# Optimization experiments

Hardware: AMD Instinct MI355X
Metric: run time of the kernel (lower is better)

The kernel has to match this reference:

```python
import jax, jax.numpy as jnp
import numpy as np

B, T, I, H, FUT = 16384, 50, 6, 128, 30


def setup_inputs() -> dict:
    key = jax.random.key(0)
    ks = jax.random.split(key, 10)
    bound = 1.0 / np.sqrt(H)
    u = lambda k, shape: jax.random.uniform(k, shape, jnp.float32, -bound, bound)
    return {
        "history": jax.random.normal(ks[0], (B, T, I), jnp.float32),
        # GRU weights (PyTorch layout: gates stacked [r, z, n])
        "w_ih": u(ks[1], (3 * H, I)),
        "w_hh": u(ks[2], (3 * H, H)),
        "b_ih": u(ks[3], (3 * H,)),
        "b_hh": u(ks[4], (3 * H,)),
        # MLP head: Linear(H,H) -> ReLU -> Linear(H,I)
        "w1": u(ks[5], (H, H)),
        "b1": u(ks[6], (H,)),
        "w2": u(ks[7], (I, H)),
        "b2": u(ks[8], (I,)),
    }


def _gru_cell(h, x, w_ih, w_hh, b_ih, b_hh):
    # PyTorch GRU cell: gates ordered r, z, n
    gi = x @ w_ih.T + b_ih          # (B, 3H)
    gh = h @ w_hh.T + b_hh          # (B, 3H)
    i_r, i_z, i_n = jnp.split(gi, 3, axis=-1)
    h_r, h_z, h_n = jnp.split(gh, 3, axis=-1)
    r = jax.nn.sigmoid(i_r + h_r)
    z = jax.nn.sigmoid(i_z + h_z)
    n = jnp.tanh(i_n + r * h_n)
    return (1.0 - z) * n + z * h


def reference(history, w_ih, w_hh, b_ih, b_hh, w1, b1, w2, b2):
    # --- encode history: scan GRU over time ---
    h0 = jnp.zeros((history.shape[0], H), history.dtype)

    def enc_step(h, x_t):
        return _gru_cell(h, x_t, w_ih, w_hh, b_ih, b_hh), None

    h_last, _ = jax.lax.scan(enc_step, h0, jnp.swapaxes(history, 0, 1))  # (B, H)

    def head(h):
        return jax.nn.relu(h @ w1.T + b1) @ w2.T + b2  # (B, I)

    def dec_step(carry, _):
        h, x = carry
        h = _gru_cell(h, x, w_ih, w_hh, b_ih, b_hh)
        x = head(h)
        return (h, x), x

    x0 = history[:, -1]  # (B, I)
    _, preds = jax.lax.scan(dec_step, (h_last, x0), None, length=FUT)  # (FUT, B, I)
    return jnp.swapaxes(preds, 0, 1)  # (B, FUT, I)
```

## Files before the change

### kernel.cpp

```cpp
#include <hip/hip_runtime.h>

typedef _Float16 half8 __attribute__((ext_vector_type(8)));
typedef float f32x4 __attribute__((ext_vector_type(4)));

#define ROWS 64
#define HP 136
#define HBUFSZ (ROWS * HP)
#define OP 184
#define LOG2E 1.442695041f
#define MFMA(a,b,c) __builtin_amdgcn_mfma_f32_16x16x32_f16((a),(b),(c),0,0,0)

__global__ __launch_bounds__(512, 2)
void traj_gru(const float* __restrict__ history,
              const float* __restrict__ w_ih, const float* __restrict__ w_hh,
              const float* __restrict__ b_ih, const float* __restrict__ b_hh,
              const float* __restrict__ w1, const float* __restrict__ b1,
              const float* __restrict__ w2, const float* __restrict__ b2,
              float* __restrict__ out)
{
    __shared__ __align__(16) _Float16 hbuf[2 * HBUFSZ];
    __shared__ __align__(16) unsigned char xo_u[50 * ROWS * 16];
    __shared__ __align__(16) _Float16 xdec[ROWS * 8];
    __shared__ __align__(16) _Float16 a1s[ROWS * HP];
    __shared__ __align__(16) _Float16 w2f[4 * 4 * 16 * 8];

    _Float16* xhist = (_Float16*)xo_u;
    float*    outs  = (float*)xo_u;

    const int tid  = threadIdx.x;
    const int wave = tid >> 6;
    const int lane = tid & 63;
    const int ln16 = lane & 15;
    const int q    = lane >> 4;
    const int sw   = ln16 & 3;
    const int rowbase = blockIdx.x * ROWS;
    const int cbase = wave * 16;
    const int bblk  = wave >> 1;
    const int colin = ((wave & 1) << 4) | ln16;

    for (int i = tid; i < 2 * HBUFSZ; i += 512) hbuf[i] = (_Float16)0;
    for (int i = tid; i < ROWS * 8; i += 512) xdec[i] = (_Float16)0;
    for (int i = tid; i < 4 * 4 * 16 * 8; i += 512) w2f[i] = (_Float16)0;
    __syncthreads();
    for (int idx = tid; idx < ROWS * 300; idx += 512) {
        int r = idx / 300, rem = idx - r * 300;
        int t = rem / 6, c = rem - t * 6;
        xhist[(t * ROWS + r) * 8 + c] = (_Float16)history[(rowbase + r) * 300 + rem];
    }
    for (int idx = tid; idx < 50 * ROWS; idx += 512) xhist[idx * 8 + 6] = (_Float16)1.0f;
    for (int idx = tid; idx < ROWS; idx += 512)      xdec[idx * 8 + 6] = (_Float16)1.0f;
    for (int idx = tid; idx < 6 * 128; idx += 512) {
        int n = idx >> 7, k = idx & 127;
        int kt = k >> 5, qq = (k >> 3) & 3, j = k & 7;
        w2f[((kt * 4 + qq) * 16 + n) * 8 + j] = (_Float16)w2[n * 128 + k];
    }

    half8 Bh[3][4];
    #pragma unroll
    for (int g = 0; g < 3; ++g) {
        float sc = (g < 2) ? -LOG2E : -2.0f * LOG2E;
        #pragma unroll
        for (int kt = 0; kt < 4; ++kt) {
            int n = g * 128 + cbase + ln16;
            const float* p = w_hh + n * 128 + kt * 32 + q * 8;
            half8 v;
            #pragma unroll
            for (int j = 0; j < 8; ++j) v[j] = (_Float16)(p[j] * sc);
            Bh[g][kt] = v;
        }
    }
    half8 Bi[3];
    #pragma unroll
    for (int g = 0; g < 3; ++g) {
        float sc = (g < 2) ? -LOG2E : -2.0f * LOG2E;
        int n = g * 128 + cbase + ln16;
        half8 v;
        #pragma unroll
        for (int j = 0; j < 8; ++j) v[j] = (_Float16)0.0f;
        if (q == 0) {
            #pragma unroll
            for (int j = 0; j < 6; ++j) v[j] = (_Float16)(w_ih[n * 6 + j] * sc);
            v[6] = (_Float16)((b_ih[n] + (g < 2 ? b_hh[n] : 0.0f)) * sc);
        }
        Bi[g] = v;
    }
    const float bhn = b_hh[256 + cbase + ln16] * (-2.0f * LOG2E);
    half8 Bw1[4];
    #pragma unroll
    for (int kt = 0; kt < 4; ++kt) {
        int n = cbase + ln16;
        const float* p = w1 + n * 128 + kt * 32 + q * 8;
        half8 v;
        #pragma unroll
        for (int j = 0; j < 8; ++j) v[j] = (_Float16)p[j];
        Bw1[kt] = v;
    }
    const float b1r = b1[cbase + ln16];
    const float b2r = (ln16 < 6) ? b2[ln16] : 0.0f;

    float hp[4][4] = {};

    __syncthreads();

    auto gru_step = [&](int p, const _Float16* xp) {
        const _Float16* hb = hbuf + p * HBUFSZ;
        _Float16*       hn = hbuf + (p ^ 1) * HBUFSZ;
        half8 Ah[2][4], Ax[2];
        f32x4 ar[2], az[2], ahh[2], an[2];

        auto loadA = [&](int c, int buf) {
            const _Float16* rp = hb + (c * 16 + ln16) * HP;
            #pragma unroll
            for (int kt = 0; kt < 4; ++kt)
                Ah[buf][kt] = *(const half8*)(rp + ((kt ^ sw) << 5) + q * 8);
            half8 x = {0,0,0,0,0,0,0,0};
            if (q == 0) x = *(const half8*)(xp + (c * 16 + ln16) * 8);
            Ax[buf] = x;
        };
        auto mfmas = [&](int buf) {
            f32x4 r = {0,0,0,0}, z = {0,0,0,0}, hh = {0,0,0,0}, n = {0,0,0,0};
            #pragma unroll
            for (int kt = 0; kt < 4; ++kt) {
                r  = MFMA(Ah[buf][kt], Bh[0][kt], r);
                z  = MFMA(Ah[buf][kt], Bh[1][kt], z);
                hh = MFMA(Ah[buf][kt], Bh[2][kt], hh);
            }
            r = MFMA(Ax[buf], Bi[0], r);
            z = MFMA(Ax[buf], Bi[1], z);
            n = MFMA(Ax[buf], Bi[2], n);
            ar[buf] = r; az[buf] = z; ahh[buf] = hh; an[buf] = n;
        };

        loadA(0, 0); mfmas(0);
        #pragma unroll
        for (int c = 0; c < 4; ++c) {
            const int cb = c & 1;
            if (c < 3) { loadA(c + 1, cb ^ 1); mfmas(cb ^ 1); }
            #pragma unroll
            for (int i = 0; i < 4; ++i) {
                float r = __builtin_amdgcn_rcpf(1.0f + __builtin_amdgcn_exp2f(ar[cb][i]));
                float z = __builtin_amdgcn_rcpf(1.0f + __builtin_amdgcn_exp2f(az[cb][i]));
                float t = an[cb][i] + r * (ahh[cb][i] + bhn);
                float n = 2.0f * __builtin_amdgcn_rcpf(1.0f + __builtin_amdgcn_exp2f(t)) - 1.0f;
                float h = n + z * (hp[c][i] - n);
                hp[c][i] = h;
                hn[(c * 16 + q * 4 + i) * HP + ((bblk ^ i) << 5) + colin] = (_Float16)h;
            }
        }
        __syncthreads();
    };

    auto head_step = [&](int f, int p) {
        const _Float16* hb = hbuf + p * HBUFSZ;
        half8 Ah[2][4];
        f32x4 aa[2];
        auto loadA = [&](int c, int buf) {
            const _Float16* rp = hb + (c * 16 + ln16) * HP;
            #pragma unroll
            for (int kt = 0; kt < 4; ++kt)
                Ah[buf][kt] = *(const half8*)(rp + ((kt ^ sw) << 5) + q * 8);
        };
        auto mfh = [&](int buf) {
            f32x4 a = {0,0,0,0};
            #pragma unroll
            for (int kt = 0; kt < 4; ++kt) a = MFMA(Ah[buf][kt], Bw1[kt], a);
            aa[buf] = a;
        };
        loadA(0, 0); mfh(0);
        #pragma unroll
        for (int c = 0; c < 4; ++c) {
            const int cb = c & 1;
            if (c < 3) { loadA(c + 1, cb ^ 1); mfh(cb ^ 1); }
            #pragma unroll
            for (int i = 0; i < 4; ++i) {
                float v = aa[cb][i] + b1r;
                v = v > 0.0f ? v : 0.0f;
                a1s[(c * 16 + q * 4 + i) * HP + ((bblk ^ i) << 5) + colin] = (_Float16)v;
            }
        }
        __syncthreads();
        if (wave < 4) {
            const _Float16* rp = a1s + (wave * 16 + ln16) * HP;
            f32x4 o = {0,0,0,0};
            #pragma unroll
            for (int kt = 0; kt < 4; ++kt) {
                half8 Aa = *(const half8*)(rp + ((kt ^ sw) << 5) + q * 8);
                half8 Bw = *(const half8*)&w2f[((kt * 4 + q) * 16 + ln16) * 8];
                o = MFMA(Aa, Bw, o);
            }
            if (ln16 < 6) {
                #pragma unroll
                for (int i = 0; i < 4; ++i) {
                    int row = wave * 16 + q * 4 + i;
                    float v = o[i] + b2r;
                    outs[row * OP + f * 6 + ln16] = v;
                    xdec[row * 8 + ln16] = (_Float16)v;
                }
            }
        }
        __syncthreads();
    };

    int p = 0;
    #pragma unroll 1
    for (int t = 0; t < 50; ++t) { gru_step(p, xhist + t * ROWS * 8); p ^= 1; }
    #pragma unroll 1
    for (int f = 0; f < 30; ++f) {
        gru_step(p, f == 0 ? xhist + 49 * ROWS * 8 : xdec);
        p ^= 1;
        head_step(f, p);
    }

    for (int idx = tid; idx < ROWS * 180; idx += 512) {
        int r = idx / 180, j = idx - r * 180;
        out[(rowbase + r) * 180 + j] = outs[r * OP + j];
    }
}

extern "C" void kernel_launch(void* const* d_in, const int* in_sizes, int n_in,
                              void* d_out, int out_size, void* d_ws, size_t ws_size,
                              hipStream_t stream) {
    (void)in_sizes; (void)n_in; (void)d_ws; (void)ws_size; (void)out_size;
    traj_gru<<<dim3(16384 / ROWS), dim3(512), 0, stream>>>(
        (const float*)d_in[0], (const float*)d_in[1], (const float*)d_in[2],
        (const float*)d_in[3], (const float*)d_in[4], (const float*)d_in[5],
        (const float*)d_in[6], (const float*)d_in[7], (const float*)d_in[8],
        (float*)d_out);
}
```

Measured before the change: 282.0 us.

## Shrink LDS footprint, fold biases into accumulators, write outputs directly

Drops the separate a1s buffer and reuses the idle half of the h double buffer for the head activations. Stores history packed at 6 halves per row and moves the GRU biases into the MFMA accumulator initial values. Writes predictions straight to global memory instead of staging them in LDS. Raises the launch-bounds occupancy hint from 2 to 4 blocks. The goal is less LDS use so more blocks fit per CU, but the tighter register budget that hint implies can force spills, and the direct global stores are small and strided.

Result: slower. 909.6 us (+222.5%).

```diff
diff --git a/kernel.cpp b/kernel.cpp
--- a/kernel.cpp
+++ b/kernel.cpp
@@ -2,15 +2,15 @@
 
 typedef _Float16 half8 __attribute__((ext_vector_type(8)));
 typedef float f32x4 __attribute__((ext_vector_type(4)));
+typedef int int4v __attribute__((ext_vector_type(4)));
 
 #define ROWS 64
 #define HP 136
 #define HBUFSZ (ROWS * HP)
-#define OP 184
 #define LOG2E 1.442695041f
 #define MFMA(a,b,c) __builtin_amdgcn_mfma_f32_16x16x32_f16((a),(b),(c),0,0,0)
 
-__global__ __launch_bounds__(512, 2)
+__global__ __launch_bounds__(512, 4)
 void traj_gru(const float* __restrict__ history,
               const float* __restrict__ w_ih, const float* __restrict__ w_hh,
               const float* __restrict__ b_ih, const float* __restrict__ b_hh,
@@ -19,13 +19,9 @@
               float* __restrict__ out)
 {
     __shared__ __align__(16) _Float16 hbuf[2 * HBUFSZ];
-    __shared__ __align__(16) unsigned char xo_u[50 * ROWS * 16];
+    __shared__ __align__(16) _Float16 xhist[50 * ROWS * 6];
     __shared__ __align__(16) _Float16 xdec[ROWS * 8];
-    __shared__ __align__(16) _Float16 a1s[ROWS * HP];
     __shared__ __align__(16) _Float16 w2f[4 * 4 * 16 * 8];
-
-    _Float16* xhist = (_Float16*)xo_u;
-    float*    outs  = (float*)xo_u;
 
     const int tid  = threadIdx.x;
     const int wave = tid >> 6;
@@ -45,10 +41,8 @@
     for (int idx = tid; idx < ROWS * 300; idx += 512) {
         int r = idx / 300, rem = idx - r * 300;
         int t = rem / 6, c = rem - t * 6;
-        xhist[(t * ROWS + r) * 8 + c] = (_Float16)history[(rowbase + r) * 300 + rem];
-    }
-    for (int idx = tid; idx < 50 * ROWS; idx += 512) xhist[idx * 8 + 6] = (_Float16)1.0f;
-    for (int idx = tid; idx < ROWS; idx += 512)      xdec[idx * 8 + 6] = (_Float16)1.0f;
+        xhist[(t * ROWS + r) * 6 + c] = (_Float16)history[(rowbase + r) * 300 + rem];
+    }
     for (int idx = tid; idx < 6 * 128; idx += 512) {
         int n = idx >> 7, k = idx & 127;
         int kt = k >> 5, qq = (k >> 3) & 3, j = k & 7;
@@ -80,10 +74,12 @@
         if (q == 0) {
             #pragma unroll
             for (int j = 0; j < 6; ++j) v[j] = (_Float16)(w_ih[n * 6 + j] * sc);
-            v[6] = (_Float16)((b_ih[n] + (g < 2 ? b_hh[n] : 0.0f)) * sc);
         }
         Bi[g] = v;
     }
+    const float brr = (b_ih[      cbase + ln16] + b_hh[      cbase + ln16]) * (-LOG2E);
+    const float brz = (b_ih[128 + cbase + ln16] + b_hh[128 + cbase + ln16]) * (-LOG2E);
+    const float bin = b_ih[256 + cbase + ln16] * (-2.0f * LOG2E);
     const float bhn = b_hh[256 + cbase + ln16] * (-2.0f * LOG2E);
     half8 Bw1[4];
     #pragma unroll
@@ -102,7 +98,7 @@
 
     __syncthreads();
 
-    auto gru_step = [&](int p, const _Float16* xp) {
+    auto gru_step = [&](int p, int t, bool enc) {
         const _Float16* hb = hbuf + p * HBUFSZ;
         _Float16*       hn = hbuf + (p ^ 1) * HBUFSZ;
         half8 Ah[2][4], Ax[2];
@@ -114,11 +110,21 @@
             for (int kt = 0; kt < 4; ++kt)
                 Ah[buf][kt] = *(const half8*)(rp + ((kt ^ sw) << 5) + q * 8);
             half8 x = {0,0,0,0,0,0,0,0};
-            if (q == 0) x = *(const half8*)(xp + (c * 16 + ln16) * 8);
+            if (q == 0) {
+                if (enc) {
+                    const int* xi = (const int*)xhist;
+                    int base = (t * ROWS + c * 16 + ln16) * 3;
+                    int4v d = { xi[base], xi[base + 1], xi[base + 2], 0 };
+                    x = __builtin_bit_cast(half8, d);
+                } else {
+                    x = *(const half8*)(xdec + (c * 16 + ln16) * 8);
+                }
+            }
             Ax[buf] = x;
         };
         auto mfmas = [&](int buf) {
-            f32x4 r = {0,0,0,0}, z = {0,0,0,0}, hh = {0,0,0,0}, n = {0,0,0,0};
+            f32x4 r = {brr,brr,brr,brr}, z = {brz,brz,brz,brz};
+            f32x4 hh = {0,0,0,0},        n = {bin,bin,bin,bin};
             #pragma unroll
             for (int kt = 0; kt < 4; ++kt) {
                 r  = MFMA(Ah[buf][kt], Bh[0][kt], r);
@@ -140,8 +146,8 @@
             for (int i = 0; i < 4; ++i) {
                 float r = __builtin_amdgcn_rcpf(1.0f + __builtin_amdgcn_exp2f(ar[cb][i]));
                 float z = __builtin_amdgcn_rcpf(1.0f + __builtin_amdgcn_exp2f(az[cb][i]));
-                float t = an[cb][i] + r * (ahh[cb][i] + bhn);
-                float n = 2.0f * __builtin_amdgcn_rcpf(1.0f + __builtin_amdgcn_exp2f(t)) - 1.0f;
+                float tt = an[cb][i] + r * (ahh[cb][i] + bhn);
+                float n = 2.0f * __builtin_amdgcn_rcpf(1.0f + __builtin_amdgcn_exp2f(tt)) - 1.0f;
                 float h = n + z * (hp[c][i] - n);
                 hp[c][i] = h;
                 hn[(c * 16 + q * 4 + i) * HP + ((bblk ^ i) << 5) + colin] = (_Float16)h;
@@ -152,6 +158,7 @@
 
     auto head_step = [&](int f, int p) {
         const _Float16* hb = hbuf + p * HBUFSZ;
+        _Float16*       a1 = hbuf + (p ^ 1) * HBUFSZ;
         half8 Ah[2][4];
         f32x4 aa[2];
         auto loadA = [&](int c, int buf) {
@@ -175,12 +182,12 @@
             for (int i = 0; i < 4; ++i) {
                 float v = aa[cb][i] + b1r;
                 v = v > 0.0f ? v : 0.0f;
-                a1s[(c * 16 + q * 4 + i) * HP + ((bblk ^ i) << 5) + colin] = (_Float16)v;
+                a1[(c * 16 + q * 4 + i) * HP + ((bblk ^ i) << 5) + colin] = (_Float16)v;
             }
         }
         __syncthreads();
         if (wave < 4) {
-            const _Float16* rp = a1s + (wave * 16 + ln16) * HP;
+            const _Float16* rp = a1 + (wave * 16 + ln16) * HP;
             f32x4 o = {0,0,0,0};
             #pragma unroll
             for (int kt = 0; kt < 4; ++kt) {
@@ -193,7 +200,7 @@
                 for (int i = 0; i < 4; ++i) {
                     int row = wave * 16 + q * 4 + i;
                     float v = o[i] + b2r;
-                    outs[row * OP + f * 6 + ln16] = v;
+                    out[(rowbase + row) * 180 + f * 6 + ln16] = v;
                     xdec[row * 8 + ln16] = (_Float16)v;
                 }
             }
@@ -203,17 +210,17 @@
 
     int p = 0;
     #pragma unroll 1
-    for (int t = 0; t < 50; ++t) { gru_step(p, xhist + t * ROWS * 8); p ^= 1; }
+    for (int t = 0; t < 50; ++t) { gru_step(p, t, true); p ^= 1; }
+    for (int idx = tid; idx < ROWS * 6; idx += 512) {
+        int r = idx / 6, c = idx - r * 6;
+        xdec[r * 8 + c] = xhist[(49 * ROWS + r) * 6 + c];
+    }
+    __syncthreads();
     #pragma unroll 1
     for (int f = 0; f < 30; ++f) {
-        gru_step(p, f == 0 ? xhist + 49 * ROWS * 8 : xdec);
+        gru_step(p, 0, false);
         p ^= 1;
         head_step(f, p);
-    }
-
-    for (int idx = tid; idx < ROWS * 180; idx += 512) {
-        int r = idx / 180, j = idx - r * 180;
-        out[(rowbase + r) * 180 + j] = outs[r * OP + j];
     }
 }
 
```
